# Optimization experiments

Hardware: AMD Instinct MI355X
Metric: run time of the kernel (lower is better)

The kernel has to match this reference:

```python
import jax, jax.numpy as jnp
import numpy as np

START_AGE = 0
END_AGE = 100
LAMBDA_1 = 0.2
LAMBDA_2 = 0.05
EPS = 1e-3

N = 524288
WIDTH = END_AGE + 1 - START_AGE  # 101


def setup_inputs() -> dict:
    key = jax.random.key(0)
    k1, k2 = jax.random.split(key)
    inp = jax.random.normal(k1, (N, WIDTH), dtype=jnp.float32)
    target = jax.random.randint(k2, (N,), 0, WIDTH, dtype=jnp.int32)
    return {"input": inp, "target": target}


def reference(input, target):
    # softmax over age bins
    p = jax.nn.softmax(input, axis=1)                                  # [N, W]
    a = jnp.arange(START_AGE, END_AGE + 1, dtype=jnp.float32)          # [W]
    tf = target.astype(jnp.float32)
    # expected age per sample
    mean = jnp.sum(p * a, axis=1)                                      # [N]
    mean_loss = jnp.mean((mean - tf) ** 2) / 2.0
    # vectorized one-hot gather: prob of ground-truth bin
    prob_gt = jnp.take_along_axis(p, target[:, None].astype(jnp.int32), axis=1)  # [N,1]
    # mask of bins with prob strictly below the GT prob; detached in the original
    mask = jax.lax.stop_gradient((p < prob_gt).astype(p.dtype))        # [N, W]
    p_not_K = mask * p
    residue_loss = jnp.mean(jnp.sum(-(p_not_K + EPS) * jnp.log(p_not_K + EPS), axis=1))
    batch_average_K = jnp.sum(mask == 0).astype(jnp.float32) / N
    return (LAMBDA_1 * mean_loss, LAMBDA_2 * residue_loss, batch_average_K)
```

## Files before the change

kernel.cpp:

```cpp
#include <hip/hip_runtime.h>

#define N_ROWS   524288
#define W_BINS   101
#define EPS_F    1e-3f
#define RPB      64
#define NBLK     (N_ROWS / RPB)
#define TILE_F   (RPB * W_BINS)
#define THREADS  256

typedef const float __attribute__((address_space(1)))* gptr_t;
typedef float __attribute__((address_space(3)))* sptr_t;

__global__ __launch_bounds__(THREADS) void mrl_main(const float* __restrict__ x,
                                                    const int* __restrict__ tgt,
                                                    float4* __restrict__ partial) {
    __shared__ float  sm[TILE_F];
    __shared__ float4 wsum[4];
    const int tid = threadIdx.x;
    const int wv  = tid >> 6;
    const float* gbase = x + (size_t)blockIdx.x * TILE_F;

    #pragma unroll
    for (int q = 0; q < 6; ++q) {
        __builtin_amdgcn_global_load_lds((gptr_t)(gbase + q * 1024 + tid * 4),
                                         (sptr_t)(sm + q * 1024 + (wv << 8)), 16, 0, 0);
    }
    if (tid < 80) {
        __builtin_amdgcn_global_load_lds((gptr_t)(gbase + 6144 + tid * 4),
                                         (sptr_t)(sm + 6144 + (wv << 8)), 16, 0, 0);
    }

    const int r = (wv << 4) | (tid & 15);
    const int h = (tid >> 4) & 3;
    const int t = tgt[blockIdx.x * RPB + r];

    __syncthreads();

    const int cb = (h == 0) ? 0 : (h * 25 + 1);
    const float* rp = sm + r * W_BINS + cb;

    float e[25];
    float e25 = 0.f;
    float se0 = 0.f, se1 = 0.f, sa0 = 0.f, sa1 = 0.f, eg = 0.f;
    #pragma unroll
    for (int i = 0; i < 24; i += 2) {
        float E0 = __expf(rp[i]);
        float E1 = __expf(rp[i + 1]);
        e[i] = E0; e[i + 1] = E1;
        se0 += E0; sa0 += E0 * (float)(cb + i);
        se1 += E1; sa1 += E1 * (float)(cb + i + 1);
        eg = (cb + i     == t) ? E0 : eg;
        eg = (cb + i + 1 == t) ? E1 : eg;
    }
    {
        float E = __expf(rp[24]);
        e[24] = E;
        se0 += E; sa0 += E * (float)(cb + 24);
        eg = (cb + 24 == t) ? E : eg;
    }
    if (h == 0) {
        e25 = __expf(rp[25]);
        se1 += e25; sa1 += e25 * 25.0f;
        eg = (t == 25) ? e25 : eg;
    }
    float se  = se0 + se1;
    float sea = sa0 + sa1;

    se  += __shfl_xor(se, 16);  se  += __shfl_xor(se, 32);
    sea += __shfl_xor(sea, 16); sea += __shfl_xor(sea, 32);
    eg  += __shfl_xor(eg, 16);  eg  += __shfl_xor(eg, 32);
    const float egt = eg;
    const float inv = __builtin_amdgcn_rcpf(se);

    float sq = 0.f;
    if (h == 0) {
        float d = sea * inv - (float)t;
        sq = d * d;
    }

    float rc0 = 0.f, rc1 = 0.f;
    int   k   = 0;
    #pragma unroll
    for (int i = 0; i < 24; i += 2) {
        float E0 = e[i], E1 = e[i + 1];
        bool  l0 = E0 < egt, l1 = E1 < egt;
        float q0 = (l0 ? E0 * inv : 0.f) + EPS_F;
        float q1 = (l1 ? E1 * inv : 0.f) + EPS_F;
        rc0 -= q0 * __logf(q0);
        rc1 -= q1 * __logf(q1);
        k   += (l0 ? 0 : 1) + (l1 ? 0 : 1);
    }
    {
        float E = e[24];
        bool  l = E < egt;
        float q = (l ? E * inv : 0.f) + EPS_F;
        rc0 -= q * __logf(q);
        k   += l ? 0 : 1;
    }
    if (h == 0) {
        bool  l = e25 < egt;
        float q = (l ? e25 * inv : 0.f) + EPS_F;
        rc1 -= q * __logf(q);
        k   += l ? 0 : 1;
    }
    float rc = rc0 + rc1;
    float kf = (float)k;

    #pragma unroll
    for (int off = 32; off >= 1; off >>= 1) {
        sq += __shfl_xor(sq, off);
        rc += __shfl_xor(rc, off);
        kf += __shfl_xor(kf, off);
    }
    if ((tid & 63) == 0) wsum[wv] = make_float4(sq, rc, kf, 0.f);
    __syncthreads();
    if (tid == 0) {
        float4 a = wsum[0], b = wsum[1], c = wsum[2], d = wsum[3];
        partial[blockIdx.x] = make_float4(a.x + b.x + c.x + d.x,
                                          a.y + b.y + c.y + d.y,
                                          a.z + b.z + c.z + d.z, 0.f);
    }
}

__global__ __launch_bounds__(1024) void mrl_reduce(const float4* __restrict__ partial,
                                                   float* __restrict__ out) {
    double s = 0.0, r = 0.0, k = 0.0;
    #pragma unroll
    for (int i = 0; i < 8; ++i) {
        float4 v = partial[threadIdx.x + (i << 10)];
        s += (double)v.x; r += (double)v.y; k += (double)v.z;
    }
    #pragma unroll
    for (int off = 32; off >= 1; off >>= 1) {
        s += __shfl_xor(s, off);
        r += __shfl_xor(r, off);
        k += __shfl_xor(k, off);
    }
    __shared__ double sd[48];
    const int w = threadIdx.x >> 6;
    if ((threadIdx.x & 63) == 0) { sd[w * 3 + 0] = s; sd[w * 3 + 1] = r; sd[w * 3 + 2] = k; }
    __syncthreads();
    if (threadIdx.x == 0) {
        double S = 0.0, R = 0.0, K = 0.0;
        #pragma unroll
        for (int i = 0; i < 16; ++i) { S += sd[i * 3]; R += sd[i * 3 + 1]; K += sd[i * 3 + 2]; }
        const double n = (double)N_ROWS;
        out[0] = (float)(0.1  * (S / n));
        out[1] = (float)(0.05 * (R / n));
        out[2] = (float)(K / n);
    }
}

extern "C" void kernel_launch(void* const* d_in, const int* in_sizes, int n_in,
                              void* d_out, int out_size, void* d_ws, size_t ws_size,
                              hipStream_t stream) {
    const float* x   = (const float*)d_in[0];
    const int*   tgt = (const int*)d_in[1];
    float*  out     = (float*)d_out;
    float4* partial = (float4*)d_ws;

    mrl_main<<<NBLK, THREADS, 0, stream>>>(x, tgt, partial);
    mrl_reduce<<<1, 1024, 0, stream>>>(partial, out);
}
```

Before: 292.3 us.

## Split block tile into two halves and overlap second load with first compute

New measurement: 293.2 us. About the same (+0.3%).

```diff
diff --git a/kernel.cpp b/kernel.cpp
--- a/kernel.cpp
+++ b/kernel.cpp
@@ -6,6 +6,7 @@
 #define RPB      64
 #define NBLK     (N_ROWS / RPB)
 #define TILE_F   (RPB * W_BINS)
+#define PHASE_F  (TILE_F / 2)
 #define THREADS  256
 
 typedef const float __attribute__((address_space(1)))* gptr_t;
@@ -16,96 +17,109 @@
                                                     float4* __restrict__ partial) {
     __shared__ float  sm[TILE_F];
     __shared__ float4 wsum[4];
-    const int tid = threadIdx.x;
-    const int wv  = tid >> 6;
+    const int tid  = threadIdx.x;
+    const int wv   = tid >> 6;
+    const int lane = tid & 63;
+    const int rl   = lane & 7;
+    const int h    = lane >> 3;
     const float* gbase = x + (size_t)blockIdx.x * TILE_F;
 
     #pragma unroll
-    for (int q = 0; q < 6; ++q) {
+    for (int q = 0; q < 3; ++q) {
         __builtin_amdgcn_global_load_lds((gptr_t)(gbase + q * 1024 + tid * 4),
                                          (sptr_t)(sm + q * 1024 + (wv << 8)), 16, 0, 0);
     }
-    if (tid < 80) {
-        __builtin_amdgcn_global_load_lds((gptr_t)(gbase + 6144 + tid * 4),
-                                         (sptr_t)(sm + 6144 + (wv << 8)), 16, 0, 0);
+    if (tid < 40) {
+        __builtin_amdgcn_global_load_lds((gptr_t)(gbase + 3072 + tid * 4),
+                                         (sptr_t)(sm + 3072), 16, 0, 0);
     }
 
-    const int r = (wv << 4) | (tid & 15);
-    const int h = (tid >> 4) & 3;
-    const int t = tgt[blockIdx.x * RPB + r];
+    const int rbase = blockIdx.x * RPB + (wv << 3) + rl;
+    const int t0 = tgt[rbase];
+    const int t1 = tgt[rbase + 32];
+
+    const int  cb    = (h < 5) ? h * 13 : 65 + (h - 5) * 12;
+    const bool extra = (h < 5);
+
+    float acc_sq = 0.f, acc_rc = 0.f;
+    int   acc_k  = 0;
+
+    auto do_phase = [&](int p, int t) {
+        const float* rp = sm + p * PHASE_F + ((wv << 3) + rl) * W_BINS + cb;
+
+        float e[13];
+        float se0 = 0.f, se1 = 0.f, sa0 = 0.f, sa1 = 0.f, eg = 0.f;
+        #pragma unroll
+        for (int i = 0; i < 12; i += 2) {
+            float E0 = __expf(rp[i]);
+            float E1 = __expf(rp[i + 1]);
+            e[i] = E0; e[i + 1] = E1;
+            se0 += E0; sa0 += E0 * (float)(cb + i);
+            se1 += E1; sa1 += E1 * (float)(cb + i + 1);
+            eg = (cb + i     == t) ? E0 : eg;
+            eg = (cb + i + 1 == t) ? E1 : eg;
+        }
+        if (extra) {
+            float E = __expf(rp[12]); e[12] = E;
+            se0 += E; sa0 += E * (float)(cb + 12);
+            eg = (cb + 12 == t) ? E : eg;
+        }
+        float se  = se0 + se1;
+        float sea = sa0 + sa1;
+
+        se  += __shfl_xor(se, 8);  se  += __shfl_xor(se, 16);  se  += __shfl_xor(se, 32);
+        sea += __shfl_xor(sea, 8); sea += __shfl_xor(sea, 16); sea += __shfl_xor(sea, 32);
+        eg  += __shfl_xor(eg, 8);  eg  += __shfl_xor(eg, 16);  eg  += __shfl_xor(eg, 32);
+        const float egt = eg;
+        const float inv = __builtin_amdgcn_rcpf(se);
+
+        if (h == 0) {
+            float d = sea * inv - (float)t;
+            acc_sq += d * d;
+        }
+
+        float rc0 = 0.f, rc1 = 0.f;
+        int   k   = 0;
+        #pragma unroll
+        for (int i = 0; i < 12; i += 2) {
+            float E0 = e[i], E1 = e[i + 1];
+            bool  l0 = E0 < egt, l1 = E1 < egt;
+            float q0 = (l0 ? E0 * inv : 0.f) + EPS_F;
+            float q1 = (l1 ? E1 * inv : 0.f) + EPS_F;
+            rc0 -= q0 * __logf(q0);
+            rc1 -= q1 * __logf(q1);
+            k   += (l0 ? 0 : 1) + (l1 ? 0 : 1);
+        }
+        if (extra) {
+            float E = e[12];
+            bool  l = E < egt;
+            float q = (l ? E * inv : 0.f) + EPS_F;
+            rc0 -= q * __logf(q);
+            k   += l ? 0 : 1;
+        }
+        acc_rc += rc0 + rc1;
+        acc_k  += k;
+    };
 
     __syncthreads();
 
-    const int cb = (h == 0) ? 0 : (h * 25 + 1);
-    const float* rp = sm + r * W_BINS + cb;
-
-    float e[25];
-    float e25 = 0.f;
-    float se0 = 0.f, se1 = 0.f, sa0 = 0.f, sa1 = 0.f, eg = 0.f;
     #pragma unroll
-    for (int i = 0; i < 24; i += 2) {
-        float E0 = __expf(rp[i]);
-        float E1 = __expf(rp[i + 1]);
-        e[i] = E0; e[i + 1] = E1;
-        se0 += E0; sa0 += E0 * (float)(cb + i);
-        se1 += E1; sa1 += E1 * (float)(cb + i + 1);
-        eg = (cb + i     == t) ? E0 : eg;
-        eg = (cb + i + 1 == t) ? E1 : eg;
+    for (int q = 0; q < 3; ++q) {
+        __builtin_amdgcn_global_load_lds((gptr_t)(gbase + PHASE_F + q * 1024 + tid * 4),
+                                         (sptr_t)(sm + PHASE_F + q * 1024 + (wv << 8)), 16, 0, 0);
     }
-    {
-        float E = __expf(rp[24]);
-        e[24] = E;
-        se0 += E; sa0 += E * (float)(cb + 24);
-        eg = (cb + 24 == t) ? E : eg;
-    }
-    if (h == 0) {
-        e25 = __expf(rp[25]);
-        se1 += e25; sa1 += e25 * 25.0f;
-        eg = (t == 25) ? e25 : eg;
-    }
-    float se  = se0 + se1;
-    float sea = sa0 + sa1;
-
-    se  += __shfl_xor(se, 16);  se  += __shfl_xor(se, 32);
-    sea += __shfl_xor(sea, 16); sea += __shfl_xor(sea, 32);
-    eg  += __shfl_xor(eg, 16);  eg  += __shfl_xor(eg, 32);
-    const float egt = eg;
-    const float inv = __builtin_amdgcn_rcpf(se);
-
-    float sq = 0.f;
-    if (h == 0) {
-        float d = sea * inv - (float)t;
-        sq = d * d;
+    if (tid < 40) {
+        __builtin_amdgcn_global_load_lds((gptr_t)(gbase + PHASE_F + 3072 + tid * 4),
+                                         (sptr_t)(sm + PHASE_F + 3072), 16, 0, 0);
     }
 
-    float rc0 = 0.f, rc1 = 0.f;
-    int   k   = 0;
-    #pragma unroll
-    for (int i = 0; i < 24; i += 2) {
-        float E0 = e[i], E1 = e[i + 1];
-        bool  l0 = E0 < egt, l1 = E1 < egt;
-        float q0 = (l0 ? E0 * inv : 0.f) + EPS_F;
-        float q1 = (l1 ? E1 * inv : 0.f) + EPS_F;
-        rc0 -= q0 * __logf(q0);
-        rc1 -= q1 * __logf(q1);
-        k   += (l0 ? 0 : 1) + (l1 ? 0 : 1);
-    }
-    {
-        float E = e[24];
-        bool  l = E < egt;
-        float q = (l ? E * inv : 0.f) + EPS_F;
-        rc0 -= q * __logf(q);
-        k   += l ? 0 : 1;
-    }
-    if (h == 0) {
-        bool  l = e25 < egt;
-        float q = (l ? e25 * inv : 0.f) + EPS_F;
-        rc1 -= q * __logf(q);
-        k   += l ? 0 : 1;
-    }
-    float rc = rc0 + rc1;
-    float kf = (float)k;
+    do_phase(0, t0);
 
+    __syncthreads();
+
+    do_phase(1, t1);
+
+    float sq = acc_sq, rc = acc_rc, kf = (float)acc_k;
     #pragma unroll
     for (int off = 32; off >= 1; off >>= 1) {
         sq += __shfl_xor(sq, off);
```
